# Optimization experiments

Hardware: AMD Instinct MI355X
Metric: run time of the kernel (lower is better)

## Reference

```python
import jax, jax.numpy as jnp
import numpy as np

N_COMPANY, N_INDUSTRY, E = 20000, 500, 8192
CC, CI, D, H = 256, 128, 256, 4


def setup_inputs() -> dict:
    key = jax.random.key(0)
    ks = jax.random.split(key, 14)
    p = lambda k, shape: (jax.random.normal(k, shape, jnp.float32) * 0.02)
    company_x = jax.random.normal(ks[0], (N_COMPANY, CC), jnp.float32)
    industry_x = jax.random.normal(ks[1], (N_INDUSTRY, CI), jnp.float32)
    src = jax.random.randint(ks[2], (E,), 0, N_COMPANY)
    tgt = jax.random.randint(ks[3], (E,), 0, N_INDUSTRY)
    edge_index = jnp.stack([src, tgt]).astype(jnp.int64)
    return {
        "company_x": company_x,
        "industry_x": industry_x,
        "edge_index": edge_index,
        "Wc": p(ks[4], (D, CC)), "bc": jnp.zeros((D,), jnp.float32),
        "Wi": p(ks[5], (D, CI)), "bi": jnp.zeros((D,), jnp.float32),
        "w_in": p(ks[6], (3 * D, D)), "b_in": jnp.zeros((3 * D,), jnp.float32),
        "w_out": p(ks[7], (D, D)), "b_out": jnp.zeros((D,), jnp.float32),
        "gamma": jnp.ones((D,), jnp.float32), "beta": jnp.zeros((D,), jnp.float32),
    }


def reference(company_x, industry_x, edge_index, Wc, bc, Wi, bi, w_in, b_in, w_out, b_out, gamma, beta):
    company_h = company_x @ Wc.T + bc          # [N, D]
    industry_h = industry_x @ Wi.T + bi        # [M, D]
    src, tgt = edge_index[0], edge_index[1]
    e = src.shape[0]
    d = company_h.shape[-1]
    hd = d // H

    q_in = company_h[src]                      # [E, D] gather
    kv_in = industry_h[tgt]                    # [E, D] gather

    wq, wk, wv = jnp.split(w_in, 3, axis=0)
    bq, bk, bv = jnp.split(b_in, 3)
    qh = (q_in @ wq.T + bq).reshape(e, H, hd)
    kh = (kv_in @ wk.T + bk).reshape(e, H, hd)
    vh = (kv_in @ wv.T + bv).reshape(e, H, hd)

    scale = 1.0 / jnp.sqrt(jnp.float32(hd))
    scores = jnp.einsum("qhd,khd->hqk", qh * scale, kh)   # [H, E, E]
    attn = jax.nn.softmax(scores, axis=-1)
    ctx = jnp.einsum("hqk,khd->qhd", attn, vh).reshape(e, d)
    attn_out = ctx @ w_out.T + b_out                        # [E, D]

    agg = jax.ops.segment_sum(attn_out, src, num_segments=company_h.shape[0])
    counts = jax.ops.segment_sum(jnp.ones((e,), jnp.float32), src, num_segments=company_h.shape[0])
    pooled = agg / (counts[:, None] + 1e-6)

    out = company_h + pooled
    mean = out.mean(-1, keepdims=True)
    var = out.var(-1, keepdims=True)
    return (out - mean) / jnp.sqrt(var + 1e-5) * gamma + beta
```

## Files before the change

kernel.cpp:

```cpp
#include <hip/hip_runtime.h>

#define E_EDGES 8192
#define N_COMP  20000
#define N_IND   500
#define NKEYS   512

typedef short bf16x8 __attribute__((ext_vector_type(8)));
typedef float f32x4  __attribute__((ext_vector_type(4)));

static __device__ __forceinline__ unsigned short f2bf(float v) {
    unsigned u = __builtin_bit_cast(unsigned, v);
    u = (u + 0x7FFFu + ((u >> 16) & 1u)) >> 16;
    return (unsigned short)u;
}

static __device__ __forceinline__ void cvt8(const float* __restrict__ s,
                                            unsigned short* __restrict__ d) {
    float4 a = *(const float4*)s;
    float4 b = *(const float4*)(s + 4);
    bf16x8 o;
    o[0] = (short)f2bf(a.x); o[1] = (short)f2bf(a.y);
    o[2] = (short)f2bf(a.z); o[3] = (short)f2bf(a.w);
    o[4] = (short)f2bf(b.x); o[5] = (short)f2bf(b.y);
    o[6] = (short)f2bf(b.z); o[7] = (short)f2bf(b.w);
    *(bf16x8*)d = o;
}

static __device__ __forceinline__ bf16x8 cvt8r(const float* __restrict__ s) {
    float4 a = *(const float4*)s;
    float4 b = *(const float4*)(s + 4);
    bf16x8 v;
    v[0] = (short)f2bf(a.x); v[1] = (short)f2bf(a.y);
    v[2] = (short)f2bf(a.z); v[3] = (short)f2bf(a.w);
    v[4] = (short)f2bf(b.x); v[5] = (short)f2bf(b.y);
    v[6] = (short)f2bf(b.z); v[7] = (short)f2bf(b.w);
    return v;
}

#define SWZ(r)   (((r) & 7) << 4)
#define SWZ4(r)  ((((r) >> 1) & 3) << 4)

static __device__ __forceinline__ void stage_f32(const float* src, char* base,
                                                 int sr, int sc) {
    *(bf16x8*)(base + ((sr * 64 + sc * 2) ^ SWZ(sr))) = cvt8r(src);
}

__global__ __launch_bounds__(256) void prep(
    const int* __restrict__ src, const int* __restrict__ tgt,
    const float* __restrict__ Wc, const float* __restrict__ Wi,
    const float* __restrict__ w_out, const float* __restrict__ w_in,
    const float* __restrict__ bc, const float* __restrict__ bi,
    const float* __restrict__ b_in,
    float* __restrict__ csrc, float* __restrict__ ctgt,
    unsigned short* __restrict__ Wc_bf, unsigned short* __restrict__ wout_bf,
    unsigned short* __restrict__ WcT_bf, unsigned short* __restrict__ Wi_bf,
    unsigned short* __restrict__ wkv_bf, float* __restrict__ beff)
{
    const int bid = blockIdx.x, tid = threadIdx.x;
    if (bid < 32) {
        int e = bid * 256 + tid;
        atomicAdd(&csrc[src[e]], 1.0f);
        atomicAdd(&ctgt[tgt[e]], 1.0f);
    } else if (bid < 64) {
        long i = ((long)(bid - 32) * 256 + tid) * 8;
        cvt8(Wc + i, Wc_bf + i);
    } else if (bid < 96) {
        long i = ((long)(bid - 64) * 256 + tid) * 8;
        cvt8(w_out + i, wout_bf + i);
    } else if (bid < 128) {
        long o = ((long)(bid - 96) * 256 + tid) * 8;
        int c = (int)(o >> 8), d0 = (int)(o & 255);
        bf16x8 v;
#pragma unroll
        for (int j = 0; j < 8; j++) v[j] = (short)f2bf(Wc[(long)(d0 + j) * 256 + c]);
        *(bf16x8*)(WcT_bf + o) = v;
    } else if (bid < 144) {
        long i = ((long)(bid - 128) * 256 + tid) * 8;
        cvt8(Wi + i, Wi_bf + i);
    } else if (bid < 208) {
        long i = ((long)(bid - 144) * 256 + tid) * 8;
        cvt8(w_in + 65536 + i, wkv_bf + i);
    } else {
        int gi = (bid - 208) * 256 + tid;
        int e = gi >> 2, q = gi & 3;
        const float* base = (e < 256) ? bc : bi;
        const float* wr = w_in + (long)e * 256 + q * 64;
        const float* br = base + q * 64;
        float s = 0.f;
#pragma unroll
        for (int j = 0; j < 64; j += 4) {
            float4 w4 = *(const float4*)(wr + j);
            float4 b4 = *(const float4*)(br + j);
            s += w4.x * b4.x + w4.y * b4.y + w4.z * b4.z + w4.w * b4.w;
        }
        s += __shfl_xor(s, 1);
        s += __shfl_xor(s, 2);
        if (q == 0) beff[e] = s + b_in[e];
    }
}

__global__ __launch_bounds__(256) void fusedW(
    const float* __restrict__ w_in, const unsigned short* __restrict__ WcT_bf,
    const float* __restrict__ industry_x, const unsigned short* __restrict__ Wi_bf,
    const unsigned short* __restrict__ wkv_bf, const float* __restrict__ beff,
    const float* __restrict__ ctgt, const float* __restrict__ csrc,
    unsigned short* __restrict__ Wcq_bf, unsigned short* __restrict__ Kbuf,
    unsigned short* __restrict__ VTg,
    float* __restrict__ cntT, int* __restrict__ list, int* __restrict__ nlist)
{
    const int bid = blockIdx.x;
    if (bid >= 20) {
        int i = (bid - 20) * 256 + threadIdx.x;
        if (i < NKEYS) cntT[(i & 15) * 32 + (i >> 4)] = ctgt[i];
        if (i < N_COMP && csrc[i] > 0.f) {
            int k = atomicAdd(nlist, 1);
            list[k] = i;
        }
        return;
    }

    __shared__ char lds[48 * 1024];
    const int t = threadIdx.x, wv = t >> 6, lane = t & 63;
    const int g = lane >> 4, ln = lane & 15;
    const int sr = t >> 2, sc = (t & 3) * 8;

    if (bid < 4) {
        char* ab = lds;
        char* wb = lds + 4 * 1024;
        const int bm = bid * 64;
        f32x4 acc[16];
#pragma unroll
        for (int i = 0; i < 16; i++) acc[i] = (f32x4){0.f, 0.f, 0.f, 0.f};
        const float* aptr = w_in + (long)(bm + sr) * 256 + sc;
        for (int kc = 0; kc < 256; kc += 32) {
            __syncthreads();
            stage_f32(aptr + kc, ab, sr, sc);
#pragma unroll
            for (int p = 0; p < 4; p++) {
                int r = p * 64 + sr;
                *(bf16x8*)(wb + ((r * 64 + sc * 2) ^ SWZ(r))) =
                    *(const bf16x8*)(WcT_bf + (long)r * 256 + kc + sc);
            }
            __syncthreads();
            int ar = wv * 16 + ln;
            bf16x8 af = *(bf16x8*)(ab + ((ar * 64 + g * 16) ^ SWZ(ar)));
#pragma unroll
            for (int nj = 0; nj < 16; nj++) {
                int wr = nj * 16 + ln;
                bf16x8 bf = *(bf16x8*)(wb + ((wr * 64 + g * 16) ^ SWZ(wr)));
                acc[nj] = __builtin_amdgcn_mfma_f32_16x16x32_bf16(af, bf, acc[nj], 0, 0, 0);
            }
        }
#pragma unroll
        for (int nj = 0; nj < 16; nj++)
#pragma unroll
            for (int r = 0; r < 4; r++)
                Wcq_bf[(long)(bm + wv * 16 + g * 4 + r) * 256 + nj * 16 + ln] =
                    f2bf(acc[nj][r]);
        return;
    }

    const int rg = (bid - 4) >> 1, colh = (bid - 4) & 1;
    char* ab  = lds;
    char* wb1 = lds + 4 * 1024;
    char* ihb = lds + 16 * 1024;
    char* wb2 = lds;

    {
        f32x4 a1[16];
#pragma unroll
        for (int i = 0; i < 16; i++) a1[i] = (f32x4){0.f, 0.f, 0.f, 0.f};
        int arow = rg * 64 + sr; if (arow > N_IND - 1) arow = N_IND - 1;
        const float* aptr = industry_x + (long)arow * 128 + sc;
        for (int kc = 0; kc < 128; kc += 32) {
            __syncthreads();
            stage_f32(aptr + kc, ab, sr, sc);
#pragma unroll
            for (int p = 0; p < 4; p++) {
                int r = p * 64 + sr;
                *(bf16x8*)(wb1 + ((r * 64 + sc * 2) ^ SWZ(r))) =
                    *(const bf16x8*)(Wi_bf + (long)r * 128 + kc + sc);
            }
            __syncthreads();
            int ar = wv * 16 + ln;
            bf16x8 af = *(bf16x8*)(ab + ((ar * 64 + g * 16) ^ SWZ(ar)));
#pragma unroll
            for (int nj = 0; nj < 16; nj++) {
                int wr = nj * 16 + ln;
                bf16x8 bf = *(bf16x8*)(wb1 + ((wr * 64 + g * 16) ^ SWZ(wr)));
                a1[nj] = __builtin_amdgcn_mfma_f32_16x16x32_bf16(af, bf, a1[nj], 0, 0, 0);
            }
        }
        __syncthreads();
#pragma unroll
        for (int nj = 0; nj < 16; nj++)
#pragma unroll
            for (int r = 0; r < 4; r++) {
                int row = wv * 16 + g * 4 + r, col = nj * 16 + ln;
                *(unsigned short*)(ihb + ((row * 512 + col * 2) ^ SWZ(row))) =
                    f2bf(a1[nj][r]);
            }
    }
    __syncthreads();

    if (colh == 0) {
        f32x4 a2[16];
#pragma unroll
        for (int i = 0; i < 16; i++) a2[i] = (f32x4){0.f, 0.f, 0.f, 0.f};
        for (int kc = 0; kc < 256; kc += 32) {
            __syncthreads();
#pragma unroll
            for (int p = 0; p < 4; p++) {
                int r = p * 64 + sr;
                *(bf16x8*)(wb2 + ((r * 64 + sc * 2) ^ SWZ(r))) =
                    *(const bf16x8*)(wkv_bf + (long)r * 256 + kc + sc);
            }
            __syncthreads();
            int row = wv * 16 + ln;
            bf16x8 af = *(bf16x8*)(ihb + ((row * 512 + (kc + g * 8) * 2) ^ SWZ(row)));
#pragma unroll
            for (int nj = 0; nj < 16; nj++) {
                int wr = nj * 16 + ln;
                bf16x8 bf = *(bf16x8*)(wb2 + ((wr * 64 + g * 16) ^ SWZ(wr)));
                a2[nj] = __builtin_amdgcn_mfma_f32_16x16x32_bf16(af, bf, a2[nj], 0, 0, 0);
            }
        }
#pragma unroll
        for (int nj = 0; nj < 16; nj++)
#pragma unroll
            for (int r = 0; r < 4; r++) {
                int R = rg * 64 + wv * 16 + g * 4 + r, n = nj * 16 + ln;
                Kbuf[(long)R * 256 + n] = f2bf(a2[nj][r] + beff[256 + n]);
            }
    } else {
        const unsigned short* wp = wkv_bf + 65536;
        f32x4 a2[16];
#pragma unroll
        for (int i = 0; i < 16; i++) a2[i] = (f32x4){0.f, 0.f, 0.f, 0.f};
        for (int kc = 0; kc < 256; kc += 32) {
            __syncthreads();
#pragma unroll
            for (int p = 0; p < 4; p++) {
                int r = p * 64 + sr;
                *(bf16x8*)(wb2 + ((r * 64 + sc * 2) ^ SWZ(r))) =
                    *(const bf16x8*)(wp + (long)r * 256 + kc + sc);
            }
            __syncthreads();
#pragma unroll
            for (int mi = 0; mi < 4; mi++) {
                int arow = wv * 64 + mi * 16 + ln;
                bf16x8 af = *(bf16x8*)(wb2 + ((arow * 64 + g * 16) ^ SWZ(arow)));
#pragma unroll
                for (int t4 = 0; t4 < 4; t4++) {
                    int brow = t4 * 16 + ln;
                    bf16x8 bfr = *(bf16x8*)(ihb + ((brow * 512 + (kc + g * 8) * 2) ^ SWZ(brow)));
                    a2[mi * 4 + t4] = __builtin_amdgcn_mfma_f32_16x16x32_bf16(af, bfr, a2[mi * 4 + t4], 0, 0, 0);
                }
            }
        }
#pragma unroll
        for (int mi = 0; mi < 4; mi++)
#pragma unroll
            for (int t4 = 0; t4 < 4; t4++)
#pragma unroll
                for (int r = 0; r < 4; r++) {
                    int nrow = wv * 64 + mi * 16 + g * 4 + r;
                    VTg[(long)nrow * 512 + rg * 64 + t4 * 16 + ln] =
                        f2bf(a2[mi * 4 + t4][r] + beff[512 + nrow]);
                }
    }
}

__global__ __launch_bounds__(256, 2) void megattn(
    const float* __restrict__ company_x,
    const unsigned short* __restrict__ Wcq,
    const float* __restrict__ beff,
    const unsigned short* __restrict__ Kbuf,
    const unsigned short* __restrict__ VTg,
    const float* __restrict__ cntT,
    const unsigned short* __restrict__ wout,
    const float* __restrict__ b_out,
    const int* __restrict__ list, const int* __restrict__ nlist,
    float* __restrict__ pooled)
{
    const int M = *nlist;
    const int bm = blockIdx.x * 16;
    if (bm >= M) return;

    __shared__ char lds[32768];
    const int t = threadIdx.x, h = t >> 6, lane = t & 63;
    const int g = lane >> 4, ln = lane & 15;
    char* qbase = lds + h * 2048;
    char* xbase = lds + 8192;
    char* pbase = lds + 16384 + h * 4096;

    {
        int row = t >> 4, c0 = (t & 15) * 16;
        int mr = bm + row; if (mr > M - 1) mr = M - 1;
        const float* src = company_x + (long)list[mr] * 256 + c0;
        *(bf16x8*)(xbase + ((row * 512 + c0 * 2) ^ SWZ(row))) = cvt8r(src);
        *(bf16x8*)(xbase + ((row * 512 + c0 * 2 + 16) ^ SWZ(row))) = cvt8r(src + 8);
    }
    __syncthreads();

    bf16x8 qf0, qf1;
    {
        f32x4 qa[4];
#pragma unroll
        for (int i = 0; i < 4; i++) qa[i] = (f32x4){0.f, 0.f, 0.f, 0.f};
#pragma unroll
        for (int kc = 0; kc < 256; kc += 32) {
            bf16x8 af = *(bf16x8*)(xbase + ((ln * 512 + (kc + g * 8) * 2) ^ SWZ(ln)));
#pragma unroll
            for (int nj = 0; nj < 4; nj++) {
                bf16x8 bf = *(const bf16x8*)(Wcq + (long)(h * 64 + nj * 16 + ln) * 256 + kc + g * 8);
                qa[nj] = __builtin_amdgcn_mfma_f32_16x16x32_bf16(af, bf, qa[nj], 0, 0, 0);
            }
        }
#pragma unroll
        for (int nj = 0; nj < 4; nj++)
#pragma unroll
            for (int r = 0; r < 4; r++) {
                int row = g * 4 + r, col = nj * 16 + ln;
                *(unsigned short*)(qbase + ((row * 128 + col * 2) ^ SWZ(row))) =
                    f2bf((qa[nj][r] + beff[h * 64 + col]) * 0.125f);
            }
        qf0 = *(bf16x8*)(qbase + ((ln * 128 + g * 16) ^ SWZ(ln)));
        qf1 = *(bf16x8*)(qbase + ((ln * 128 + 64 + g * 16) ^ SWZ(ln)));
    }

    f32x4 acc[4];
#pragma unroll
    for (int i = 0; i < 4; i++) acc[i] = (f32x4){0.f, 0.f, 0.f, 0.f};
    float mreg[4] = {-1e30f, -1e30f, -1e30f, -1e30f};
    float lreg[4] = {0.f, 0.f, 0.f, 0.f};

#pragma unroll
    for (int tile = 0; tile < 2; tile++) {
        float cnt[16];
        {
            const float* cp = cntT + ln * 32 + tile * 16;
#pragma unroll
            for (int j4 = 0; j4 < 4; j4++) {
                float4 c4 = *(const float4*)(cp + j4 * 4);
                cnt[j4 * 4 + 0] = c4.x; cnt[j4 * 4 + 1] = c4.y;
                cnt[j4 * 4 + 2] = c4.z; cnt[j4 * 4 + 3] = c4.w;
            }
        }

        f32x4 S[8][2];
#pragma unroll
        for (int half = 0; half < 2; half++) {
            bf16x8 k0r[4][2], k1r[4][2];
#pragma unroll
            for (int c4 = 0; c4 < 4; c4++)
#pragma unroll
                for (int sub = 0; sub < 2; sub++) {
                    const unsigned short* kr = Kbuf +
                        (long)(tile * 256 + (half * 4 + c4) * 32 + sub * 16 + ln) * 256 + h * 64 + g * 8;
                    k0r[c4][sub] = *(const bf16x8*)(kr);
                    k1r[c4][sub] = *(const bf16x8*)(kr + 32);
                }
#pragma unroll
            for (int c4 = 0; c4 < 4; c4++)
#pragma unroll
                for (int sub = 0; sub < 2; sub++) {
                    f32x4 s = (f32x4){0.f, 0.f, 0.f, 0.f};
                    s = __builtin_amdgcn_mfma_f32_16x16x32_bf16(qf0, k0r[c4][sub], s, 0, 0, 0);
                    s = __builtin_amdgcn_mfma_f32_16x16x32_bf16(qf1, k1r[c4][sub], s, 0, 0, 0);
                    S[half * 4 + c4][sub] = s;
                }
        }

        bf16x8 vr[2][2][4];
#pragma unroll
        for (int j = 0; j < 2; j++)
#pragma unroll
            for (int t4 = 0; t4 < 4; t4++)
                vr[0][j][t4] = *(const bf16x8*)(
                    VTg + (long)(h * 64 + t4 * 16 + ln) * 512 + tile * 256 + j * 32 + g * 8);

        float tm[4] = {-1e30f, -1e30f, -1e30f, -1e30f};
#pragma unroll
        for (int c = 0; c < 8; c++)
#pragma unroll
            for (int sub = 0; sub < 2; sub++)
#pragma unroll
                for (int r = 0; r < 4; r++) tm[r] = fmaxf(tm[r], S[c][sub][r]);
#pragma unroll
        for (int st = 1; st < 16; st <<= 1)
#pragma unroll
            for (int r = 0; r < 4; r++) tm[r] = fmaxf(tm[r], __shfl_xor(tm[r], st));

        float corr[4];
#pragma unroll
        for (int r = 0; r < 4; r++) {
            float mn = fmaxf(mreg[r], tm[r]);
            corr[r] = __expf(mreg[r] - mn);
            mreg[r] = mn;
        }

        float ps[4] = {0.f, 0.f, 0.f, 0.f};
#pragma unroll
        for (int c = 0; c < 8; c++)
#pragma unroll
            for (int sub = 0; sub < 2; sub++) {
                float cv = cnt[c * 2 + sub];
#pragma unroll
                for (int r = 0; r < 4; r++) {
                    float p = cv * __expf(S[c][sub][r] - mreg[r]);
                    S[c][sub][r] = p;
                    ps[r] += p;
                }
            }
#pragma unroll
        for (int st = 1; st < 16; st <<= 1)
#pragma unroll
            for (int r = 0; r < 4; r++) ps[r] += __shfl_xor(ps[r], st);
#pragma unroll
        for (int r = 0; r < 4; r++) lreg[r] = lreg[r] * corr[r] + ps[r];
#pragma unroll
        for (int i = 0; i < 4; i++)
#pragma unroll
            for (int r = 0; r < 4; r++) acc[i][r] *= corr[r];

#pragma unroll
        for (int grp = 0; grp < 4; grp++) {
            if (grp < 3) {
#pragma unroll
                for (int j = 0; j < 2; j++)
#pragma unroll
                    for (int t4 = 0; t4 < 4; t4++)
                        vr[(grp + 1) & 1][j][t4] = *(const bf16x8*)(
                            VTg + (long)(h * 64 + t4 * 16 + ln) * 512 +
                            tile * 256 + ((grp + 1) * 2 + j) * 32 + g * 8);
            }
#pragma unroll
            for (int j = 0; j < 2; j++) {
                int c = grp * 2 + j;
                char* pb = pbase + (c & 3) * 1024;
#pragma unroll
                for (int sub = 0; sub < 2; sub++)
#pragma unroll
                    for (int r = 0; r < 4; r++) {
                        int row = g * 4 + r;
                        *(unsigned short*)(pb + ((row * 64 + (sub * 16 + ln) * 2) ^ SWZ4(row))) =
                            f2bf(S[c][sub][r]);
                    }
                bf16x8 pa = *(bf16x8*)(pb + ((ln * 64 + g * 16) ^ SWZ4(ln)));
#pragma unroll
                for (int t4 = 0; t4 < 4; t4++)
                    acc[t4] = __builtin_amdgcn_mfma_f32_16x16x32_bf16(
                        pa, vr[grp & 1][j][t4], acc[t4], 0, 0, 0);
            }
        }
    }

#pragma unroll
    for (int t4 = 0; t4 < 4; t4++)
#pragma unroll
        for (int r = 0; r < 4; r++) {
            int row = g * 4 + r, col = t4 * 16 + ln;
            *(unsigned short*)(qbase + ((row * 128 + col * 2) ^ SWZ(row))) =
                f2bf(acc[t4][r] / lreg[r]);
        }
    __syncthreads();

    {
        f32x4 oa[4];
#pragma unroll
        for (int i = 0; i < 4; i++) oa[i] = (f32x4){0.f, 0.f, 0.f, 0.f};
#pragma unroll
        for (int kc = 0; kc < 256; kc += 32) {
            int hs = kc >> 6;
            int off = (kc & 63) + g * 8;
            bf16x8 af = *(bf16x8*)(lds + hs * 2048 + ((ln * 128 + off * 2) ^ SWZ(ln)));
#pragma unroll
            for (int nj = 0; nj < 4; nj++) {
                bf16x8 bf = *(const bf16x8*)(wout + (long)(h * 64 + nj * 16 + ln) * 256 + kc + g * 8);
                oa[nj] = __builtin_amdgcn_mfma_f32_16x16x32_bf16(af, bf, oa[nj], 0, 0, 0);
            }
        }
#pragma unroll
        for (int nj = 0; nj < 4; nj++) {
            int n = h * 64 + nj * 16 + ln;
            float bv = b_out[n];
#pragma unroll
            for (int r = 0; r < 4; r++) {
                int R = bm + g * 4 + r;
                if (R < M)
                    pooled[(long)list[R] * 256 + n] = oa[nj][r] + bv;
            }
        }
    }
}

__global__ __launch_bounds__(256) void gemm_ln(
    const float* __restrict__ A, const unsigned short* __restrict__ W,
    const float* __restrict__ bias,
    const float* __restrict__ pooled, const float* __restrict__ csrc,
    const float* __restrict__ gamma, const float* __restrict__ beta,
    float* __restrict__ out, int M, int K)
{
    __shared__ unsigned short As[64 * 32];
    __shared__ unsigned short Ws[256 * 32];
    char* abase = (char*)As;
    char* wbase = (char*)Ws;

    const int bm = blockIdx.x * 64;
    const int t = threadIdx.x;
    const int wv = t >> 6, lane = t & 63, g = lane >> 4, ln = lane & 15;

    f32x4 acc[16];
#pragma unroll
    for (int i = 0; i < 16; i++) acc[i] = (f32x4){0.f, 0.f, 0.f, 0.f};

    const int sr = t >> 2;
    const int sc = (t & 3) * 8;
    int arow = bm + sr; if (arow > M - 1) arow = M - 1;
    const float* aptr = A + (long)arow * K + sc;

    for (int kc = 0; kc < K; kc += 32) {
        __syncthreads();
        stage_f32(aptr + kc, abase, sr, sc);
#pragma unroll
        for (int p = 0; p < 4; p++) {
            int r = p * 64 + sr;
            *(bf16x8*)(wbase + ((r * 64 + sc * 2) ^ SWZ(r))) =
                *(const bf16x8*)(W + (long)r * K + kc + sc);
        }
        __syncthreads();

        const int ar = wv * 16 + ln;
        bf16x8 af = *(bf16x8*)(abase + ((ar * 64 + g * 16) ^ SWZ(ar)));
#pragma unroll
        for (int nj = 0; nj < 16; nj++) {
            int wr = nj * 16 + ln;
            bf16x8 bf = *(bf16x8*)(wbase + ((wr * 64 + g * 16) ^ SWZ(wr)));
            acc[nj] = __builtin_amdgcn_mfma_f32_16x16x32_bf16(af, bf, acc[nj], 0, 0, 0);
        }
    }

#pragma unroll
    for (int r = 0; r < 4; r++) {
        int R = bm + wv * 16 + g * 4 + r;
        bool valid = R < M;
        int Rc = valid ? R : 0;
        float cntv = csrc[Rc];
        float factor = (valid && cntv > 0.f) ? cntv / (cntv + 1e-6f) : 0.f;

        float v[16];
        float sum = 0.f, sq = 0.f;
#pragma unroll
        for (int nj = 0; nj < 16; nj++) {
            int n = nj * 16 + ln;
            float x = acc[nj][r] + bias[n] + factor * pooled[(long)Rc * 256 + n];
            v[nj] = x;
            sum += x;
            sq  += x * x;
        }
#pragma unroll
        for (int st = 1; st < 16; st <<= 1) {
            sum += __shfl_xor(sum, st);
            sq  += __shfl_xor(sq,  st);
        }
        float mean = sum * (1.0f / 256.0f);
        float var  = sq * (1.0f / 256.0f) - mean * mean;
        float rstd = rsqrtf(var + 1e-5f);
        if (valid) {
#pragma unroll
            for (int nj = 0; nj < 16; nj++) {
                int n = nj * 16 + ln;
                out[(long)R * 256 + n] = (v[nj] - mean) * rstd * gamma[n] + beta[n];
            }
        }
    }
}

extern "C" void kernel_launch(void* const* d_in, const int* in_sizes, int n_in,
                              void* d_out, int out_size, void* d_ws, size_t ws_size,
                              hipStream_t stream)
{
    const float* company_x  = (const float*)d_in[0];
    const float* industry_x = (const float*)d_in[1];
    const int*   edge       = (const int*)d_in[2];
    const float* Wc         = (const float*)d_in[3];
    const float* bc         = (const float*)d_in[4];
    const float* Wi         = (const float*)d_in[5];
    const float* bi         = (const float*)d_in[6];
    const float* w_in       = (const float*)d_in[7];
    const float* b_in       = (const float*)d_in[8];
    const float* w_out      = (const float*)d_in[9];
    const float* b_out      = (const float*)d_in[10];
    const float* gamma      = (const float*)d_in[11];
    const float* beta       = (const float*)d_in[12];
    float* out = (float*)d_out;

    const int* src = edge;
    const int* tgt = edge + E_EDGES;

    float* wf = (float*)d_ws;
    size_t o = 0;
    unsigned short* Wc_bf   = (unsigned short*)(wf + o); o += 32768;
    unsigned short* wout_bf = (unsigned short*)(wf + o); o += 32768;
    unsigned short* WcT_bf  = (unsigned short*)(wf + o); o += 32768;
    unsigned short* Wi_bf   = (unsigned short*)(wf + o); o += 16384;
    unsigned short* wkv_bf  = (unsigned short*)(wf + o); o += 65536;
    unsigned short* Wcq_bf  = (unsigned short*)(wf + o); o += 32768;
    unsigned short* Kbuf    = (unsigned short*)(wf + o); o += 65536;
    unsigned short* VTg     = (unsigned short*)(wf + o); o += 65536;
    float* pooled           = wf + o; o += (size_t)N_COMP * 256;
    float* beff             = wf + o; o += 768;
    float* cntT             = wf + o; o += NKEYS;
    int*   list             = (int*)(wf + o); o += E_EDGES;
    float* csrc             = wf + o; o += N_COMP;
    float* ctgt             = wf + o; o += NKEYS;
    int*   nlist            = (int*)(wf + o); o += 4;

    hipMemsetAsync(csrc, 0, (N_COMP + NKEYS + 4) * sizeof(float), stream);

    prep<<<dim3(220), dim3(256), 0, stream>>>(
        src, tgt, Wc, Wi, w_out, w_in, bc, bi, b_in,
        csrc, ctgt, Wc_bf, wout_bf, WcT_bf, Wi_bf, wkv_bf, beff);

    fusedW<<<dim3(99), dim3(256), 0, stream>>>(
        w_in, WcT_bf, industry_x, Wi_bf, wkv_bf, beff, ctgt, csrc,
        Wcq_bf, Kbuf, VTg, cntT, list, nlist);

    megattn<<<dim3(E_EDGES / 16), dim3(256), 0, stream>>>(
        company_x, Wcq_bf, beff, Kbuf, VTg, cntT, wout_bf, b_out,
        list, nlist, pooled);

    gemm_ln<<<dim3((N_COMP + 63) / 64), dim3(256), 0, stream>>>(
        company_x, Wc_bf, bc, pooled, csrc, gamma, beta, out, N_COMP, 256);
}
```

Baseline: 102.6 us.

## Fuse attention, company projection and LayerNorm into one kernel over all rows

Drops the compacted list of source companies and the separate pooled buffer and gemm_ln kernel. A single kernel now handles every company row in 16-row blocks: it computes the company projection and the query projection together, runs attention against the per-target keys, applies the output projection, then does a LayerNorm reduced across waves in LDS. This removes a launch, the atomic list build and the 20 MB pooled write and read. In exchange it does attention work for all 20000 rows, including rows with no edges, instead of only the roughly 8000 that appear as sources.

```diff
diff --git a/kernel.cpp b/kernel.cpp
--- a/kernel.cpp
+++ b/kernel.cpp
@@ -103,19 +103,14 @@
     const float* __restrict__ w_in, const unsigned short* __restrict__ WcT_bf,
     const float* __restrict__ industry_x, const unsigned short* __restrict__ Wi_bf,
     const unsigned short* __restrict__ wkv_bf, const float* __restrict__ beff,
-    const float* __restrict__ ctgt, const float* __restrict__ csrc,
+    const float* __restrict__ ctgt,
     unsigned short* __restrict__ Wcq_bf, unsigned short* __restrict__ Kbuf,
-    unsigned short* __restrict__ VTg,
-    float* __restrict__ cntT, int* __restrict__ list, int* __restrict__ nlist)
+    unsigned short* __restrict__ VTg, float* __restrict__ cntT)
 {
     const int bid = blockIdx.x;
     if (bid >= 20) {
         int i = (bid - 20) * 256 + threadIdx.x;
         if (i < NKEYS) cntT[(i & 15) * 32 + (i >> 4)] = ctgt[i];
-        if (i < N_COMP && csrc[i] > 0.f) {
-            int k = atomicAdd(nlist, 1);
-            list[k] = i;
-        }
         return;
     }
 
@@ -271,8 +266,10 @@
     }
 }
 
-__global__ __launch_bounds__(256, 2) void megattn(
+__global__ __launch_bounds__(256, 2) void mega(
     const float* __restrict__ company_x,
+    const unsigned short* __restrict__ Wc_bf,
+    const float* __restrict__ bc,
     const unsigned short* __restrict__ Wcq,
     const float* __restrict__ beff,
     const unsigned short* __restrict__ Kbuf,
@@ -280,53 +277,59 @@
     const float* __restrict__ cntT,
     const unsigned short* __restrict__ wout,
     const float* __restrict__ b_out,
-    const int* __restrict__ list, const int* __restrict__ nlist,
-    float* __restrict__ pooled)
+    const float* __restrict__ csrc,
+    const float* __restrict__ gamma, const float* __restrict__ beta,
+    float* __restrict__ out)
 {
-    const int M = *nlist;
     const int bm = blockIdx.x * 16;
-    if (bm >= M) return;
-
-    __shared__ char lds[32768];
+    __shared__ char lds[33280];
     const int t = threadIdx.x, h = t >> 6, lane = t & 63;
     const int g = lane >> 4, ln = lane & 15;
-    char* qbase = lds + h * 2048;
-    char* xbase = lds + 8192;
-    char* pbase = lds + 16384 + h * 4096;
+    char* xbase   = lds;
+    char* ctxbase = lds + 8192;
+    char* pbase   = lds + 16384 + h * 4096;
+    float* psum   = (float*)(lds + 32768);
+    float* psq    = psum + 64;
 
     {
         int row = t >> 4, c0 = (t & 15) * 16;
-        int mr = bm + row; if (mr > M - 1) mr = M - 1;
-        const float* src = company_x + (long)list[mr] * 256 + c0;
+        const float* src = company_x + (long)(bm + row) * 256 + c0;
         *(bf16x8*)(xbase + ((row * 512 + c0 * 2) ^ SWZ(row))) = cvt8r(src);
         *(bf16x8*)(xbase + ((row * 512 + c0 * 2 + 16) ^ SWZ(row))) = cvt8r(src + 8);
     }
     __syncthreads();
 
+    f32x4 ch[4], qa[4];
+#pragma unroll
+    for (int i = 0; i < 4; i++) {
+        ch[i] = (f32x4){0.f, 0.f, 0.f, 0.f};
+        qa[i] = (f32x4){0.f, 0.f, 0.f, 0.f};
+    }
+#pragma unroll
+    for (int kc = 0; kc < 256; kc += 32) {
+        bf16x8 af = *(bf16x8*)(xbase + ((ln * 512 + (kc + g * 8) * 2) ^ SWZ(ln)));
+#pragma unroll
+        for (int nj = 0; nj < 4; nj++) {
+            long wrow = (long)(h * 64 + nj * 16 + ln) * 256 + kc + g * 8;
+            bf16x8 b1 = *(const bf16x8*)(Wc_bf + wrow);
+            bf16x8 b2 = *(const bf16x8*)(Wcq + wrow);
+            ch[nj] = __builtin_amdgcn_mfma_f32_16x16x32_bf16(af, b1, ch[nj], 0, 0, 0);
+            qa[nj] = __builtin_amdgcn_mfma_f32_16x16x32_bf16(af, b2, qa[nj], 0, 0, 0);
+        }
+    }
+
     bf16x8 qf0, qf1;
     {
-        f32x4 qa[4];
-#pragma unroll
-        for (int i = 0; i < 4; i++) qa[i] = (f32x4){0.f, 0.f, 0.f, 0.f};
-#pragma unroll
-        for (int kc = 0; kc < 256; kc += 32) {
-            bf16x8 af = *(bf16x8*)(xbase + ((ln * 512 + (kc + g * 8) * 2) ^ SWZ(ln)));
-#pragma unroll
-            for (int nj = 0; nj < 4; nj++) {
-                bf16x8 bf = *(const bf16x8*)(Wcq + (long)(h * 64 + nj * 16 + ln) * 256 + kc + g * 8);
-                qa[nj] = __builtin_amdgcn_mfma_f32_16x16x32_bf16(af, bf, qa[nj], 0, 0, 0);
-            }
-        }
 #pragma unroll
         for (int nj = 0; nj < 4; nj++)
 #pragma unroll
             for (int r = 0; r < 4; r++) {
                 int row = g * 4 + r, col = nj * 16 + ln;
-                *(unsigned short*)(qbase + ((row * 128 + col * 2) ^ SWZ(row))) =
+                *(unsigned short*)(pbase + ((row * 128 + col * 2) ^ SWZ(row))) =
                     f2bf((qa[nj][r] + beff[h * 64 + col]) * 0.125f);
             }
-        qf0 = *(bf16x8*)(qbase + ((ln * 128 + g * 16) ^ SWZ(ln)));
-        qf1 = *(bf16x8*)(qbase + ((ln * 128 + 64 + g * 16) ^ SWZ(ln)));
+        qf0 = *(bf16x8*)(pbase + ((ln * 128 + g * 16) ^ SWZ(ln)));
+        qf1 = *(bf16x8*)(pbase + ((ln * 128 + 64 + g * 16) ^ SWZ(ln)));
     }
 
     f32x4 acc[4];
@@ -372,13 +375,11 @@
                 }
         }
 
-        bf16x8 vr[2][2][4];
-#pragma unroll
-        for (int j = 0; j < 2; j++)
-#pragma unroll
-            for (int t4 = 0; t4 < 4; t4++)
-                vr[0][j][t4] = *(const bf16x8*)(
-                    VTg + (long)(h * 64 + t4 * 16 + ln) * 512 + tile * 256 + j * 32 + g * 8);
+        bf16x8 vr[2][4];
+#pragma unroll
+        for (int t4 = 0; t4 < 4; t4++)
+            vr[0][t4] = *(const bf16x8*)(
+                VTg + (long)(h * 64 + t4 * 16 + ln) * 512 + tile * 256 + g * 8);
 
         float tm[4] = {-1e30f, -1e30f, -1e30f, -1e30f};
 #pragma unroll
@@ -425,34 +426,28 @@
             for (int r = 0; r < 4; r++) acc[i][r] *= corr[r];
 
 #pragma unroll
-        for (int grp = 0; grp < 4; grp++) {
-            if (grp < 3) {
-#pragma unroll
-                for (int j = 0; j < 2; j++)
-#pragma unroll
-                    for (int t4 = 0; t4 < 4; t4++)
-                        vr[(grp + 1) & 1][j][t4] = *(const bf16x8*)(
-                            VTg + (long)(h * 64 + t4 * 16 + ln) * 512 +
-                            tile * 256 + ((grp + 1) * 2 + j) * 32 + g * 8);
-            }
-#pragma unroll
-            for (int j = 0; j < 2; j++) {
-                int c = grp * 2 + j;
-                char* pb = pbase + (c & 3) * 1024;
-#pragma unroll
-                for (int sub = 0; sub < 2; sub++)
-#pragma unroll
-                    for (int r = 0; r < 4; r++) {
-                        int row = g * 4 + r;
-                        *(unsigned short*)(pb + ((row * 64 + (sub * 16 + ln) * 2) ^ SWZ4(row))) =
-                            f2bf(S[c][sub][r]);
-                    }
-                bf16x8 pa = *(bf16x8*)(pb + ((ln * 64 + g * 16) ^ SWZ4(ln)));
+        for (int c = 0; c < 8; c++) {
+            if (c < 7) {
 #pragma unroll
                 for (int t4 = 0; t4 < 4; t4++)
-                    acc[t4] = __builtin_amdgcn_mfma_f32_16x16x32_bf16(
-                        pa, vr[grp & 1][j][t4], acc[t4], 0, 0, 0);
-            }
+                    vr[(c + 1) & 1][t4] = *(const bf16x8*)(
+                        VTg + (long)(h * 64 + t4 * 16 + ln) * 512 +
+                        tile * 256 + (c + 1) * 32 + g * 8);
+            }
+            char* pb = pbase + (c & 1) * 1024;
+#pragma unroll
+            for (int sub = 0; sub < 2; sub++)
+#pragma unroll
+                for (int r = 0; r < 4; r++) {
+                    int row = g * 4 + r;
+                    *(unsigned short*)(pb + ((row * 64 + (sub * 16 + ln) * 2) ^ SWZ4(row))) =
+                        f2bf(S[c][sub][r]);
+                }
+            bf16x8 pa = *(bf16x8*)(pb + ((ln * 64 + g * 16) ^ SWZ4(ln)));
+#pragma unroll
+            for (int t4 = 0; t4 < 4; t4++)
+                acc[t4] = __builtin_amdgcn_mfma_f32_16x16x32_bf16(
+                    pa, vr[c & 1][t4], acc[t4], 0, 0, 0);
         }
     }
 
@@ -460,119 +455,67 @@
     for (int t4 = 0; t4 < 4; t4++)
 #pragma unroll
         for (int r = 0; r < 4; r++) {
-            int row = g * 4 + r, col = t4 * 16 + ln;
-            *(unsigned short*)(qbase + ((row * 128 + col * 2) ^ SWZ(row))) =
+            int row = g * 4 + r, col = h * 64 + t4 * 16 + ln;
+            *(unsigned short*)(ctxbase + ((row * 512 + col * 2) ^ SWZ(row))) =
                 f2bf(acc[t4][r] / lreg[r]);
         }
     __syncthreads();
 
-    {
-        f32x4 oa[4];
-#pragma unroll
-        for (int i = 0; i < 4; i++) oa[i] = (f32x4){0.f, 0.f, 0.f, 0.f};
-#pragma unroll
-        for (int kc = 0; kc < 256; kc += 32) {
-            int hs = kc >> 6;
-            int off = (kc & 63) + g * 8;
-            bf16x8 af = *(bf16x8*)(lds + hs * 2048 + ((ln * 128 + off * 2) ^ SWZ(ln)));
-#pragma unroll
-            for (int nj = 0; nj < 4; nj++) {
-                bf16x8 bf = *(const bf16x8*)(wout + (long)(h * 64 + nj * 16 + ln) * 256 + kc + g * 8);
-                oa[nj] = __builtin_amdgcn_mfma_f32_16x16x32_bf16(af, bf, oa[nj], 0, 0, 0);
-            }
-        }
+    f32x4 oa[4];
+#pragma unroll
+    for (int i = 0; i < 4; i++) oa[i] = (f32x4){0.f, 0.f, 0.f, 0.f};
+#pragma unroll
+    for (int kc = 0; kc < 256; kc += 32) {
+        bf16x8 af = *(bf16x8*)(ctxbase + ((ln * 512 + (kc + g * 8) * 2) ^ SWZ(ln)));
+#pragma unroll
+        for (int nj = 0; nj < 4; nj++) {
+            bf16x8 bf = *(const bf16x8*)(wout + (long)(h * 64 + nj * 16 + ln) * 256 + kc + g * 8);
+            oa[nj] = __builtin_amdgcn_mfma_f32_16x16x32_bf16(af, bf, oa[nj], 0, 0, 0);
+        }
+    }
+
+    float v[4][4];
+#pragma unroll
+    for (int r = 0; r < 4; r++) {
+        int R = bm + g * 4 + r;
+        float cntv = csrc[R];
+        float factor = (cntv > 0.f) ? cntv / (cntv + 1e-6f) : 0.f;
+        float s = 0.f, sq = 0.f;
 #pragma unroll
         for (int nj = 0; nj < 4; nj++) {
             int n = h * 64 + nj * 16 + ln;
-            float bv = b_out[n];
-#pragma unroll
-            for (int r = 0; r < 4; r++) {
-                int R = bm + g * 4 + r;
-                if (R < M)
-                    pooled[(long)list[R] * 256 + n] = oa[nj][r] + bv;
-            }
-        }
-    }
-}
-
-__global__ __launch_bounds__(256) void gemm_ln(
-    const float* __restrict__ A, const unsigned short* __restrict__ W,
-    const float* __restrict__ bias,
-    const float* __restrict__ pooled, const float* __restrict__ csrc,
-    const float* __restrict__ gamma, const float* __restrict__ beta,
-    float* __restrict__ out, int M, int K)
-{
-    __shared__ unsigned short As[64 * 32];
-    __shared__ unsigned short Ws[256 * 32];
-    char* abase = (char*)As;
-    char* wbase = (char*)Ws;
-
-    const int bm = blockIdx.x * 64;
-    const int t = threadIdx.x;
-    const int wv = t >> 6, lane = t & 63, g = lane >> 4, ln = lane & 15;
-
-    f32x4 acc[16];
-#pragma unroll
-    for (int i = 0; i < 16; i++) acc[i] = (f32x4){0.f, 0.f, 0.f, 0.f};
-
-    const int sr = t >> 2;
-    const int sc = (t & 3) * 8;
-    int arow = bm + sr; if (arow > M - 1) arow = M - 1;
-    const float* aptr = A + (long)arow * K + sc;
-
-    for (int kc = 0; kc < K; kc += 32) {
-        __syncthreads();
-        stage_f32(aptr + kc, abase, sr, sc);
-#pragma unroll
-        for (int p = 0; p < 4; p++) {
-            int r = p * 64 + sr;
-            *(bf16x8*)(wbase + ((r * 64 + sc * 2) ^ SWZ(r))) =
-                *(const bf16x8*)(W + (long)r * K + kc + sc);
-        }
-        __syncthreads();
-
-        const int ar = wv * 16 + ln;
-        bf16x8 af = *(bf16x8*)(abase + ((ar * 64 + g * 16) ^ SWZ(ar)));
-#pragma unroll
-        for (int nj = 0; nj < 16; nj++) {
-            int wr = nj * 16 + ln;
-            bf16x8 bf = *(bf16x8*)(wbase + ((wr * 64 + g * 16) ^ SWZ(wr)));
-            acc[nj] = __builtin_amdgcn_mfma_f32_16x16x32_bf16(af, bf, acc[nj], 0, 0, 0);
-        }
-    }
+            float x = ch[nj][r] + bc[n] + factor * (oa[nj][r] + b_out[n]);
+            v[r][nj] = x;
+            s += x;
+            sq += x * x;
+        }
+#pragma unroll
+        for (int st = 1; st < 16; st <<= 1) {
+            s  += __shfl_xor(s,  st);
+            sq += __shfl_xor(sq, st);
+        }
+        if (ln == 0) {
+            psum[(g * 4 + r) * 4 + h] = s;
+            psq[(g * 4 + r) * 4 + h]  = sq;
+        }
+    }
+    __syncthreads();
 
 #pragma unroll
     for (int r = 0; r < 4; r++) {
-        int R = bm + wv * 16 + g * 4 + r;
-        bool valid = R < M;
-        int Rc = valid ? R : 0;
-        float cntv = csrc[Rc];
-        float factor = (valid && cntv > 0.f) ? cntv / (cntv + 1e-6f) : 0.f;
-
-        float v[16];
-        float sum = 0.f, sq = 0.f;
-#pragma unroll
-        for (int nj = 0; nj < 16; nj++) {
-            int n = nj * 16 + ln;
-            float x = acc[nj][r] + bias[n] + factor * pooled[(long)Rc * 256 + n];
-            v[nj] = x;
-            sum += x;
-            sq  += x * x;
-        }
-#pragma unroll
-        for (int st = 1; st < 16; st <<= 1) {
-            sum += __shfl_xor(sum, st);
-            sq  += __shfl_xor(sq,  st);
-        }
-        float mean = sum * (1.0f / 256.0f);
-        float var  = sq * (1.0f / 256.0f) - mean * mean;
+        int row = g * 4 + r;
+        int R = bm + row;
+        float tot  = psum[row * 4 + 0] + psum[row * 4 + 1] +
+                     psum[row * 4 + 2] + psum[row * 4 + 3];
+        float totq = psq[row * 4 + 0] + psq[row * 4 + 1] +
+                     psq[row * 4 + 2] + psq[row * 4 + 3];
+        float mean = tot * (1.0f / 256.0f);
+        float var  = totq * (1.0f / 256.0f) - mean * mean;
         float rstd = rsqrtf(var + 1e-5f);
-        if (valid) {
-#pragma unroll
-            for (int nj = 0; nj < 16; nj++) {
-                int n = nj * 16 + ln;
-                out[(long)R * 256 + n] = (v[nj] - mean) * rstd * gamma[n] + beta[n];
-            }
+#pragma unroll
+        for (int nj = 0; nj < 4; nj++) {
+            int n = h * 64 + nj * 16 + ln;
+            out[(long)R * 256 + n] = (v[r][nj] - mean) * rstd * gamma[n] + beta[n];
         }
     }
 }
@@ -609,28 +552,22 @@
     unsigned short* Wcq_bf  = (unsigned short*)(wf + o); o += 32768;
     unsigned short* Kbuf    = (unsigned short*)(wf + o); o += 65536;
     unsigned short* VTg     = (unsigned short*)(wf + o); o += 65536;
-    float* pooled           = wf + o; o += (size_t)N_COMP * 256;
     float* beff             = wf + o; o += 768;
     float* cntT             = wf + o; o += NKEYS;
-    int*   list             = (int*)(wf + o); o += E_EDGES;
     float* csrc             = wf + o; o += N_COMP;
     float* ctgt             = wf + o; o += NKEYS;
-    int*   nlist            = (int*)(wf + o); o += 4;
-
-    hipMemsetAsync(csrc, 0, (N_COMP + NKEYS + 4) * sizeof(float), stream);
+
+    hipMemsetAsync(csrc, 0, (N_COMP + NKEYS) * sizeof(float), stream);
 
     prep<<<dim3(220), dim3(256), 0, stream>>>(
         src, tgt, Wc, Wi, w_out, w_in, bc, bi, b_in,
         csrc, ctgt, Wc_bf, wout_bf, WcT_bf, Wi_bf, wkv_bf, beff);
 
-    fusedW<<<dim3(99), dim3(256), 0, stream>>>(
-        w_in, WcT_bf, industry_x, Wi_bf, wkv_bf, beff, ctgt, csrc,
-        Wcq_bf, Kbuf, VTg, cntT, list, nlist);
-
-    megattn<<<dim3(E_EDGES / 16), dim3(256), 0, stream>>>(
-        company_x, Wcq_bf, beff, Kbuf, VTg, cntT, wout_bf, b_out,
-        list, nlist, pooled);
-
-    gemm_ln<<<dim3((N_COMP + 63) / 64), dim3(256), 0, stream>>>(
-        company_x, Wc_bf, bc, pooled, csrc, gamma, beta, out, N_COMP, 256);
-}
+    fusedW<<<dim3(22), dim3(256), 0, stream>>>(
+        w_in, WcT_bf, industry_x, Wi_bf, wkv_bf, beff, ctgt,
+        Wcq_bf, Kbuf, VTg, cntT);
+
+    mega<<<dim3(N_COMP / 16), dim3(256), 0, stream>>>(
+        company_x, Wc_bf, bc, Wcq_bf, beff, Kbuf, VTg, cntT,
+        wout_bf, b_out, csrc, gamma, beta, out);
+}
```

Result: slower. 166.2 us (+62.0%).
